# Performance work log

Measured on AMD Instinct MI355X. Metric: run time of the kernel, lower is better.

## Reference

```python
import jax, jax.numpy as jnp
import numpy as np

B, T, D, H = 2, 2048, 1024, 16
DH = D // H
PD = 6
SCALE = DH ** -0.5
_PAIRS4 = [(0, 1), (0, 2), (0, 3), (1, 2), (1, 3), (2, 3)]
_J6 = jnp.array([[0, 0, 0, 0, 0, 1], [0, 0, 0, 0, -1, 0], [0, 0, 0, 1, 0, 0],
                 [0, 0, 1, 0, 0, 0], [0, -1, 0, 0, 0, 0], [1, 0, 0, 0, 0, 0]], dtype=jnp.float32)


def exterior(p1, p2):
    # p1, p2: (..., 4) -> normalized 6-d Plucker line (..., 6)
    parts = [p1[..., i] * p2[..., j] - p1[..., j] * p2[..., i] for i, j in _PAIRS4]
    L = jnp.stack(parts, axis=-1)
    n = jnp.linalg.norm(L, axis=-1, keepdims=True)
    return L / jnp.clip(n, 1e-12)


def setup_inputs() -> dict:
    key = jax.random.key(0)
    ks = jax.random.split(key, 12)
    s = 0.02
    return {
        'x': jax.random.normal(ks[0], (B, T, D), jnp.float32),
        'qkv_w': jax.random.normal(ks[1], (D, 3 * D), jnp.float32) * s,
        'qkv_b': jnp.zeros((3 * D,), jnp.float32),
        'w1_write': jax.random.normal(ks[2], (D, 4 * H), jnp.float32) * s,
        'w2_write': jax.random.normal(ks[3], (D, 4 * H), jnp.float32) * s,
        'w1_read': jax.random.normal(ks[4], (D, 4 * H), jnp.float32) * s,
        'w2_read': jax.random.normal(ks[5], (D, 4 * H), jnp.float32) * s,
        'memv_w': jax.random.normal(ks[6], (D, D), jnp.float32) * s,
        'memv_b': jnp.zeros((D,), jnp.float32),
        'memg_w': jax.random.normal(ks[7], (D, H), jnp.float32) * s,
        'memg_b': jnp.zeros((H,), jnp.float32),
        'mem_scale': jnp.full((H,), 0.1, jnp.float32),
        'rw_mix': jnp.zeros((), jnp.float32),
        'out_w': jax.random.normal(ks[8], (D, D), jnp.float32) * s,
        'out_b': jnp.zeros((D,), jnp.float32),
        'decay_logits': jnp.full((H,), 4.6, jnp.float32),
    }


def reference(x, qkv_w, qkv_b, w1_write, w2_write, w1_read, w2_read,
              memv_w, memv_b, memg_w, memg_b, mem_scale, rw_mix,
              out_w, out_b, decay_logits):
    # ---- standard causal softmax attention ----
    qkv = (x @ qkv_w + qkv_b).reshape(B, T, 3, H, DH).transpose(2, 0, 3, 1, 4)
    q, k, v = qkv[0], qkv[1], qkv[2]                      # each (B,H,T,DH)
    scores = jnp.einsum('bhtd,bhsd->bhts', q, k) * SCALE
    mask = jnp.triu(jnp.ones((T, T), bool), 1)
    scores = jnp.where(mask[None, None], -jnp.inf, scores)
    attn = jax.nn.softmax(scores, axis=-1)                # dropout=0 (eval)
    seq_out = jnp.einsum('bhts,bhsd->bthd', attn, v).reshape(B, T, D)

    # ---- Plucker lines for write (prev->cur) and read ----
    x_prev = jnp.concatenate([jnp.zeros((B, 1, D), x.dtype), x[:, :-1]], axis=1)
    w1 = (x_prev @ w1_write).reshape(B, T, H, 4)
    w2 = (x @ w2_write).reshape(B, T, H, 4)
    write_lines = exterior(w1, w2)                        # (B,T,H,6)
    r1 = (x @ w1_read).reshape(B, T, H, 4)
    r2 = (x @ w2_read).reshape(B, T, H, 4)
    read_lines = exterior(r1, r2)

    Jw = jnp.einsum('bthi,ij->bhtj', write_lines, _J6)    # (B,H,T,6)
    Jr = jnp.einsum('bthi,ij->bhtj', read_lines, _J6)
    rd = read_lines.transpose(0, 2, 1, 3)                 # (B,H,T,6)

    # ---- decay-weighted cumsum of 6x6 outer-product states ----
    decays = jax.nn.sigmoid(decay_logits)                 # (H,)
    pos = jnp.arange(T, dtype=x.dtype)
    decay_inv = (1.0 / jnp.clip(decays, 1e-6))[:, None] ** pos[None]   # (H,T)
    decay_fwd = decays[:, None] ** pos[None]                           # (H,T)

    def shifted_state(Jv):
        outer = Jv[..., :, None] * Jv[..., None, :]       # (B,H,T,6,6)
        ow = outer * decay_inv[None, :, :, None, None]
        M = jnp.cumsum(ow, axis=2)
        M = jnp.concatenate([jnp.zeros((B, H, 1, PD, PD), x.dtype), M[:, :, :-1]], axis=2)
        return M * decay_fwd[None, :, :, None, None]

    Mw = shifted_state(Jw)
    Mr = shifted_state(Jr)

    score_w = jnp.einsum('bhti,bhtij,bhtj->bht', rd, Mw, rd)
    score_r = jnp.einsum('bhti,bhtij,bhtj->bht', Jw, Mr, Jw)
    alpha = jax.nn.sigmoid(rw_mix)
    mem_score = (1 - alpha) * score_w + alpha * score_r   # (B,H,T)

    mem_val = x @ memv_w + memv_b                         # (B,T,D)
    gate = jax.nn.sigmoid(x @ memg_w + memg_b)            # (B,T,H)
    mem_score_t = mem_score.transpose(0, 2, 1)            # (B,T,H)
    gated = jax.nn.sigmoid(mem_score_t * mem_scale[None, None, :]) * gate
    gated = gated.mean(axis=-1, keepdims=True)            # (B,T,1)

    return (seq_out + gated * mem_val) @ out_w + out_b
```

## Files before the change

### kernel.cpp

```cpp
#include <hip/hip_runtime.h>

#define Bb 2
#define Tt 2048
#define Dd 1024
#define Hh 16
#define LDC 4480

typedef __attribute__((ext_vector_type(8))) short s16x8;
typedef __attribute__((ext_vector_type(4))) float f32x4;
typedef __attribute__((ext_vector_type(8))) _Float16 f16x8;

__device__ __forceinline__ float bf2f(unsigned short u) {
  unsigned v = ((unsigned)u) << 16;
  union { unsigned u; float f; } c; c.u = v; return c.f;
}
__device__ __forceinline__ unsigned short f2bf(float f) {
  union { float f; unsigned u; } c; c.f = f;
  unsigned u = c.u + 0x7fffu + ((c.u >> 16) & 1u);
  return (unsigned short)(u >> 16);
}
__device__ __forceinline__ float sigm(float x) { return 1.f / (1.f + expf(-x)); }

__device__ __forceinline__ int swz(int row, int k) {
  return (k & ~31) | (k & 7) | (((((k >> 3) & 3) ^ ((row >> 1) & 3))) << 3);
}

__device__ __forceinline__ void async_copy16(void* lds, const void* g) {
  __builtin_amdgcn_global_load_lds(
      (const __attribute__((address_space(1))) unsigned int*)g,
      (__attribute__((address_space(3))) unsigned int*)lds, 16, 0, 0);
}


__global__ __launch_bounds__(256) void cast_x_kernel(const float* __restrict__ x,
                                                     unsigned short* __restrict__ xb) {
  int i = blockIdx.x * 256 + threadIdx.x;
  int row = i >> 7;
  int colbase = (i & 127) * 8;
  const float4* xv = reinterpret_cast<const float4*>(x + (size_t)i * 8);
  float4 a = xv[0], b = xv[1];
  s16x8 out;
  out[0] = (short)f2bf(a.x); out[1] = (short)f2bf(a.y);
  out[2] = (short)f2bf(a.z); out[3] = (short)f2bf(a.w);
  out[4] = (short)f2bf(b.x); out[5] = (short)f2bf(b.y);
  out[6] = (short)f2bf(b.z); out[7] = (short)f2bf(b.w);
  *(s16x8*)&xb[(size_t)row * 1024 + swz(row, colbase)] = out;
}


__global__ __launch_bounds__(256) void build_wt_kernel(const float* __restrict__ qkv_w,
                                                       const float* __restrict__ w1w,
                                                       const float* __restrict__ w2w,
                                                       const float* __restrict__ w1r,
                                                       const float* __restrict__ w2r,
                                                       const float* __restrict__ memg_w,
                                                       const float* __restrict__ memv_w,
                                                       unsigned short* __restrict__ WT) {
  __shared__ float tile[32][33];
  int n0 = blockIdx.x * 32, k0 = blockIdx.y * 32;
  int tx = threadIdx.x & 31, ty = threadIdx.x >> 5;
#pragma unroll
  for (int i = 0; i < 4; i++) {
    int k = k0 + ty + i * 8, n = n0 + tx;
    float v;
    if (n < 3072)       v = qkv_w[(size_t)k * 3072 + n];
    else if (n < 3136)  v = w1w[k * 64 + (n - 3072)];
    else if (n < 3200)  v = w2w[k * 64 + (n - 3136)];
    else if (n < 3264)  v = w1r[k * 64 + (n - 3200)];
    else if (n < 3328)  v = w2r[k * 64 + (n - 3264)];
    else if (n < 3344)  v = memg_w[k * 16 + (n - 3328)];
    else if (n < 3392)  v = 0.f;
    else if (n < 4416)  v = memv_w[(size_t)k * 1024 + (n - 3392)];
    else                v = 0.f;
    tile[ty + i * 8][tx] = v;
  }
  __syncthreads();
#pragma unroll
  for (int i = 0; i < 4; i++) {
    int n = n0 + ty + i * 8, k = k0 + tx;
    WT[(size_t)n * 1024 + swz(n, k)] = f2bf(tile[tx][ty + i * 8]);
  }
}

__global__ __launch_bounds__(256) void transpose_cast_kernel(const float* __restrict__ src,
                                                             int ncols,
                                                             unsigned short* __restrict__ dst) {
  __shared__ float tile[32][33];
  int n0 = blockIdx.x * 32, k0 = blockIdx.y * 32;
  int tx = threadIdx.x & 31, ty = threadIdx.x >> 5;
#pragma unroll
  for (int i = 0; i < 4; i++) {
    int k = k0 + ty + i * 8, n = n0 + tx;
    tile[ty + i * 8][tx] = (n < ncols) ? src[(size_t)k * ncols + n] : 0.f;
  }
  __syncthreads();
#pragma unroll
  for (int i = 0; i < 4; i++) {
    int n = n0 + ty + i * 8, k = k0 + tx;
    if (n < ncols) dst[(size_t)n * 1024 + swz(n, k)] = f2bf(tile[tx][ty + i * 8]);
  }
}

__global__ void bias_fill_kernel(const float* __restrict__ qkv_b,
                                 const float* __restrict__ memg_b,
                                 const float* __restrict__ memv_b,
                                 float* __restrict__ bias) {
  int i = blockIdx.x * 256 + threadIdx.x;
  if (i >= LDC) return;
  float v = 0.f;
  if (i < 3072) v = qkv_b[i];
  else if (i >= 3328 && i < 3344) v = memg_b[i - 3328];
  else if (i >= 3392 && i < 4416) v = memv_b[i - 3392];
  bias[i] = v;
}


template <bool OUT_BF16>
__global__ __launch_bounds__(256) void gemm_kernel(const unsigned short* __restrict__ A,
                                                   const unsigned short* __restrict__ Bt,
                                                   void* __restrict__ Cout,
                                                   const float* __restrict__ bias,
                                                   int M, int N, int K) {
  __shared__ unsigned short As[128 * 32];
  __shared__ unsigned short Bs[128 * 32];
  const int tid = threadIdx.x;
  const int lane = tid & 63, wid = tid >> 6;
  const int quad = lane >> 4, c16 = lane & 15;
  const int mBase = blockIdx.y * 128, nBase = blockIdx.x * 128;
  const int wm = wid >> 1, wn = wid & 1;
  const int srow = lane >> 2, scol = (lane & 3) << 3;
  const int slot = (quad ^ ((c16 >> 1) & 3)) * 8;

  f32x4 acc[4][4] = {};
  for (int k0 = 0; k0 < K; k0 += 32) {
    __syncthreads();
#pragma unroll
    for (int j = 0; j < 2; j++) {
      int rr = wid * 32 + j * 16;
      async_copy16(&As[rr * 32], &A[(size_t)(mBase + rr + srow) * K + k0 + scol]);
      async_copy16(&Bs[rr * 32], &Bt[(size_t)(nBase + rr + srow) * K + k0 + scol]);
    }
    __syncthreads();
    s16x8 af[4], bf[4];
#pragma unroll
    for (int mt = 0; mt < 4; mt++)
      af[mt] = *(const s16x8*)&As[(wm * 64 + mt * 16 + c16) * 32 + slot];
#pragma unroll
    for (int nt = 0; nt < 4; nt++)
      bf[nt] = *(const s16x8*)&Bs[(wn * 64 + nt * 16 + c16) * 32 + slot];
#pragma unroll
    for (int mt = 0; mt < 4; mt++)
#pragma unroll
      for (int nt = 0; nt < 4; nt++)
        acc[mt][nt] = __builtin_amdgcn_mfma_f32_16x16x32_bf16(af[mt], bf[nt], acc[mt][nt], 0, 0, 0);
  }
#pragma unroll
  for (int mt = 0; mt < 4; mt++)
#pragma unroll
    for (int nt = 0; nt < 4; nt++) {
      int col = nBase + wn * 64 + nt * 16 + c16;
      float bv = bias[col];
#pragma unroll
      for (int r = 0; r < 4; r++) {
        int row = mBase + wm * 64 + mt * 16 + quad * 4 + r;
        float v = acc[mt][nt][r] + bv;
        if (OUT_BF16)
          ((unsigned short*)Cout)[(size_t)row * N + col] = f2bf(v);
        else
          ((float*)Cout)[(size_t)row * N + col] = v;
      }
    }
}


__global__ __launch_bounds__(256) void repack_kernel(const unsigned short* __restrict__ Cq,
                                                     unsigned short* __restrict__ Kt,
                                                     unsigned short* __restrict__ Vt) {
  int kb = blockIdx.x & 63, bh = blockIdx.x >> 6;
  int b = bh >> 4, h = bh & 15;
  int tid = threadIdx.x;
  size_t tbase = ((size_t)bh * 64 + kb) * 2048;
  {
    int key = tid >> 3, p = tid & 7, dg = p ^ (key & 7);
    size_t src = (size_t)(b * Tt + kb * 32 + key) * LDC + 1024 + h * 64 + dg * 8;
    s16x8 kv = *(const s16x8*)&Cq[src];
    *(s16x8*)&Kt[tbase + (size_t)tid * 8] = kv;
  }
  __shared__ unsigned short vt[32 * 66];
  {
    int row = tid >> 3, c = tid & 7;
    size_t src = (size_t)(b * Tt + kb * 32 + row) * LDC + 2048 + h * 64 + c * 8;
    s16x8 vv = *(const s16x8*)&Cq[src];
#pragma unroll
    for (int e = 0; e < 8; e++) {
      union { _Float16 hf; unsigned short s; } cv;
      cv.hf = (_Float16)bf2f((unsigned short)vv[e]);
      vt[row * 66 + c * 8 + e] = cv.s;
    }
  }
  __syncthreads();
  {
    int d = tid >> 2, p = tid & 3, cq = p ^ ((d >> 2) & 3);
    s16x8 out;
#pragma unroll
    for (int e = 0; e < 8; e++) {
      int key = ((e >> 2) & 1) * 16 + cq * 4 + (e & 3);
      out[e] = (short)vt[key * 66 + d];
    }
    *(s16x8*)&Vt[tbase + (size_t)tid * 8] = out;
  }
}


__device__ __forceinline__ void do_tile(int ks, int q0, int quad, int c16,
                                        const s16x8& qf0, const s16x8& qf1,
                                        const s16x8 kf[2][2], const f16x8 vb[4],
                                        float& l_i, f32x4 o[4]) {
  f32x4 st0 = {}, st1 = {};
  st0 = __builtin_amdgcn_mfma_f32_16x16x32_bf16(kf[0][0], qf0, st0, 0, 0, 0);
  st0 = __builtin_amdgcn_mfma_f32_16x16x32_bf16(kf[0][1], qf1, st0, 0, 0, 0);
  st1 = __builtin_amdgcn_mfma_f32_16x16x32_bf16(kf[1][0], qf0, st1, 0, 0, 0);
  st1 = __builtin_amdgcn_mfma_f32_16x16x32_bf16(kf[1][1], qf1, st1, 0, 0, 0);
  bool need_mask = (ks + 31 > q0);
  f16x8 pa;
  float lp = 0.f;
#pragma unroll
  for (int r = 0; r < 4; r++) {
    float v0 = st0[r] * 0.125f;
    float v1 = st1[r] * 0.125f;
    if (need_mask) {
      v0 = (ks + quad * 4 + r      <= q0 + c16) ? v0 : -1e30f;
      v1 = (ks + 16 + quad * 4 + r <= q0 + c16) ? v1 : -1e30f;
    }
    float p0 = __expf(v0);
    float p1 = __expf(v1);
    lp += p0 + p1;
    pa[r]     = (_Float16)p0;
    pa[4 + r] = (_Float16)p1;
  }
  l_i += lp;
#pragma unroll
  for (int nt = 0; nt < 4; nt++)
    o[nt] = __builtin_amdgcn_mfma_f32_16x16x32_f16(pa, vb[nt], o[nt], 0, 0, 0);
}

__global__ __launch_bounds__(256) void attn_kernel(const unsigned short* __restrict__ Cq,
                                                   const unsigned short* __restrict__ Kt,
                                                   const unsigned short* __restrict__ Vt,
                                                   unsigned short* __restrict__ po) {
  __shared__ unsigned short Kl[2048];
  __shared__ unsigned short Vl[2048];
  const int g0 = blockIdx.x, bh = blockIdx.y;
  const int g = ((bh >> 4) & 1) ? (15 - g0) : g0;
  const int b = bh >> 4, h = bh & 15;
  const int w = threadIdx.x >> 6, lane = threadIdx.x & 63;
  const int quad = lane >> 4, c16 = lane & 15;
  const int pi = g * 4 + w;
  const int qA = pi * 16, qB = 2032 - pi * 16;
  const int nkA = qA + 16, nkB = 2048 - pi * 16;
  const int bound = 2048 - 64 * g;
  const unsigned short* Ktb = Kt + (size_t)bh * 64 * 2048;
  const unsigned short* Vtb = Vt + (size_t)bh * 64 * 2048;
  const int ci = threadIdx.x;

  size_t rowA = (size_t)(b * Tt + qA + c16) * LDC + h * 64;
  size_t rowB = (size_t)(b * Tt + qB + c16) * LDC + h * 64;
  s16x8 qA0 = *(const s16x8*)&Cq[rowA + quad * 8];
  s16x8 qA1 = *(const s16x8*)&Cq[rowA + 32 + quad * 8];
  s16x8 qB0 = *(const s16x8*)&Cq[rowB + quad * 8];
  s16x8 qB1 = *(const s16x8*)&Cq[rowB + 32 + quad * 8];

  float lA = 0.f, lB = 0.f;
  f32x4 oA[4] = {}, oB[4] = {};

  {
    s16x8 k0 = *(const s16x8*)&Ktb[(size_t)ci * 8];
    s16x8 v0 = *(const s16x8*)&Vtb[(size_t)ci * 8];
    *(s16x8*)&Kl[ci * 8] = k0;
    *(s16x8*)&Vl[ci * 8] = v0;
  }
  __syncthreads();

  for (int ks = 0; ks < bound; ks += 32) {
    bool more = (ks + 32) < bound;
    s16x8 kreg, vreg;
    if (more) {
      size_t nb = ((size_t)(ks >> 5) + 1) * 2048 + (size_t)ci * 8;
      kreg = *(const s16x8*)&Ktb[nb];
      vreg = *(const s16x8*)&Vtb[nb];
    }
    if (ks < nkB) {
      s16x8 kf[2][2];
#pragma unroll
      for (int gg = 0; gg < 2; gg++)
#pragma unroll
        for (int half = 0; half < 2; half++) {
          int key = gg * 16 + c16;
          int p = (half * 4 + quad) ^ (c16 & 7);
          kf[gg][half] = *(const s16x8*)&Kl[(key * 8 + p) * 8];
        }
      f16x8 vb[4];
#pragma unroll
      for (int nt = 0; nt < 4; nt++) {
        int d = nt * 16 + c16;
        int p = quad ^ ((d >> 2) & 3);
        vb[nt] = *(const f16x8*)&Vl[(d * 4 + p) * 8];
      }
      do_tile(ks, qB, quad, c16, qB0, qB1, kf, vb, lB, oB);
      if (ks < nkA)
        do_tile(ks, qA, quad, c16, qA0, qA1, kf, vb, lA, oA);
    }
    __syncthreads();
    if (more) {
      *(s16x8*)&Kl[ci * 8] = kreg;
      *(s16x8*)&Vl[ci * 8] = vreg;
      __syncthreads();
    }
  }

  lB += __shfl_xor(lB, 16, 64); lB += __shfl_xor(lB, 32, 64);
  lA += __shfl_xor(lA, 16, 64); lA += __shfl_xor(lA, 32, 64);
  float invB = 1.f / lB, invA = 1.f / lA;
#pragma unroll
  for (int r = 0; r < 4; r++) {
    float ivB = __shfl(invB, quad * 4 + r, 64);
    float ivA = __shfl(invA, quad * 4 + r, 64);
    size_t baseB = (size_t)(b * Tt + qB + quad * 4 + r) * Dd + h * 64;
    size_t baseA = (size_t)(b * Tt + qA + quad * 4 + r) * Dd + h * 64;
#pragma unroll
    for (int nt = 0; nt < 4; nt++) {
      po[baseB + nt * 16 + c16] = f2bf(oB[nt][r] * ivB);
      po[baseA + nt * 16 + c16] = f2bf(oA[nt][r] * ivA);
    }
  }
}


__device__ __forceinline__ void ext6(const float* p, const float* q, float* L) {
  L[0] = p[0] * q[1] - p[1] * q[0];
  L[1] = p[0] * q[2] - p[2] * q[0];
  L[2] = p[0] * q[3] - p[3] * q[0];
  L[3] = p[1] * q[2] - p[2] * q[1];
  L[4] = p[1] * q[3] - p[3] * q[1];
  L[5] = p[2] * q[3] - p[3] * q[2];
  float n = sqrtf(L[0]*L[0] + L[1]*L[1] + L[2]*L[2] + L[3]*L[3] + L[4]*L[4] + L[5]*L[5]);
  float inv = 1.f / fmaxf(n, 1e-12f);
#pragma unroll
  for (int k = 0; k < 6; k++) L[k] *= inv;
}

__global__ void lines_kernel(const unsigned short* __restrict__ Cq,
                             float* __restrict__ Jw, float* __restrict__ Jr,
                             float* __restrict__ rd) {
  int idx = blockIdx.x * 256 + threadIdx.x;
  int h = idx & 15, t = (idx >> 4) & 2047, b = idx >> 15;
  size_t row = (size_t)(b * Tt + t) * LDC;
  float w1[4], w2[4], r1[4], r2[4];
#pragma unroll
  for (int k = 0; k < 4; k++) {
    w1[k] = (t > 0) ? bf2f(Cq[row - LDC + 3072 + h * 4 + k]) : 0.f;
    w2[k] = bf2f(Cq[row + 3136 + h * 4 + k]);
    r1[k] = bf2f(Cq[row + 3200 + h * 4 + k]);
    r2[k] = bf2f(Cq[row + 3264 + h * 4 + k]);
  }
  float Lw[6], Lr[6];
  ext6(w1, w2, Lw);
  ext6(r1, r2, Lr);
  size_t ob = ((size_t)(b * Hh + h) * Tt + t) * 6;
  Jw[ob + 0] = Lw[5]; Jw[ob + 1] = -Lw[4]; Jw[ob + 2] = Lw[3];
  Jw[ob + 3] = Lw[2]; Jw[ob + 4] = -Lw[1]; Jw[ob + 5] = Lw[0];
  Jr[ob + 0] = Lr[5]; Jr[ob + 1] = -Lr[4]; Jr[ob + 2] = Lr[3];
  Jr[ob + 3] = Lr[2]; Jr[ob + 4] = -Lr[1]; Jr[ob + 5] = Lr[0];
#pragma unroll
  for (int k = 0; k < 6; k++) rd[ob + k] = Lr[k];
}


__global__ __launch_bounds__(64) void scanA_kernel(const float* __restrict__ Jw,
                                                   const float* __restrict__ Jr,
                                                   const float* __restrict__ decay_logits,
                                                   float* __restrict__ chunkA) {
  int blk = blockIdx.x;
  int chunk = blk & 15, bh = (blk >> 4) & 31, type = blk >> 9;
  int lane = threadIdx.x;
  const float* V = (type == 0 ? Jw : Jr) + ((size_t)bh * Tt + chunk * 128) * 6;
  __shared__ float v[768];
  for (int i = lane; i < 768; i += 64) v[i] = V[i];
  __syncthreads();
  float d = sigm(decay_logits[bh & 15]);
  int ll = lane < 36 ? lane : 35;
  int i6 = ll / 6, j6 = ll % 6;
  float A = 0.f;
  for (int s = 0; s < 128; s++) A = d * A + v[s * 6 + i6] * v[s * 6 + j6];
  if (lane < 36) chunkA[((size_t)(type * 32 + bh) * 16 + chunk) * 36 + lane] = A;
}

__global__ void scanA2_kernel(const float* __restrict__ chunkA,
                              const float* __restrict__ decay_logits,
                              float* __restrict__ Bst) {
  int idx = blockIdx.x * 256 + threadIdx.x;
  if (idx >= 2 * 32 * 36) return;
  int entry = idx % 36, bh = (idx / 36) % 32, type = idx / (36 * 32);
  float d = sigm(decay_logits[bh & 15]);
  float dS = powf(d, 128.f);
  float Bv = 0.f;
  size_t base = (size_t)(type * 32 + bh) * 16;
  for (int c = 0; c < 16; c++) {
    Bst[(base + c) * 36 + entry] = Bv;
    Bv = dS * Bv + d * chunkA[(base + c) * 36 + entry];
  }
}

__global__ __launch_bounds__(128) void scanB_kernel(const float* __restrict__ Jw,
                                                    const float* __restrict__ Jr,
                                                    const float* __restrict__ rd,
                                                    const float* __restrict__ Bst,
                                                    const float* __restrict__ decay_logits,
                                                    float* __restrict__ score_w,
                                                    float* __restrict__ score_r) {
  int blk = blockIdx.x;
  int chunk = blk & 15, bh = (blk >> 4) & 31, type = blk >> 9;
  int tl = threadIdx.x;
  size_t tb = ((size_t)bh * Tt + chunk * 128) * 6;
  const float* U = (type == 0 ? rd : Jw) + tb;
  const float* W = (type == 0 ? Jw : Jr) + tb;
  __shared__ float wv[768];
  __shared__ float Bm[36];
  for (int i = tl; i < 768; i += 128) wv[i] = W[i];
  if (tl < 36) Bm[tl] = Bst[((size_t)(type * 32 + bh) * 16 + chunk) * 36 + tl];
  __syncthreads();
  float d = sigm(decay_logits[bh & 15]);
  float u[6];
#pragma unroll
  for (int i = 0; i < 6; i++) u[i] = U[tl * 6 + i];
  float q = 0.f;
#pragma unroll
  for (int i = 0; i < 6; i++) {
    float bi = 0.f;
#pragma unroll
    for (int j = 0; j < 6; j++) bi += Bm[i * 6 + j] * u[j];
    q += u[i] * bi;
  }
  float acc = 0.f;
  for (int s = 0; s < tl; s++) {
    const float* ws = &wv[s * 6];
    float dot = u[0]*ws[0] + u[1]*ws[1] + u[2]*ws[2] + u[3]*ws[3] + u[4]*ws[4] + u[5]*ws[5];
    acc = d * (acc + dot * dot);
  }
  float score = acc + powf(d, (float)tl) * q;
  float* outp = (type == 0 ? score_w : score_r);
  outp[(size_t)bh * Tt + chunk * 128 + tl] = score;
}


__global__ __launch_bounds__(256) void combine_kernel(const unsigned short* __restrict__ po,
                                                      const unsigned short* __restrict__ Cq,
                                                      const float* __restrict__ score_w,
                                                      const float* __restrict__ score_r,
                                                      const float* __restrict__ mem_scale,
                                                      const float* __restrict__ rw_mix,
                                                      unsigned short* __restrict__ fused) {
  __shared__ float tmp[16];
  int rowi = blockIdx.x;
  int b = rowi >> 11, t = rowi & 2047;
  float alpha = sigm(rw_mix[0]);
  if (threadIdx.x < 16) {
    int h = threadIdx.x;
    size_t sh = (size_t)(b * 16 + h) * Tt + t;
    float ms = (1.f - alpha) * score_w[sh] + alpha * score_r[sh];
    float gate = sigm(bf2f(Cq[(size_t)rowi * LDC + 3328 + h]));
    tmp[h] = sigm(ms * mem_scale[h]) * gate;
  }
  __syncthreads();
  float g = 0.f;
#pragma unroll
  for (int h = 0; h < 16; h++) g += tmp[h];
  g *= (1.f / 16.f);
  for (int d = threadIdx.x; d < Dd; d += 256) {
    float sv = bf2f(po[((size_t)b * Tt + t) * Dd + d]);
    float mv = bf2f(Cq[(size_t)rowi * LDC + 3392 + d]);
    fused[(size_t)rowi * Dd + swz(rowi, d)] = f2bf(sv + g * mv);
  }
}


extern "C" void kernel_launch(void* const* d_in, const int* in_sizes, int n_in,
                              void* d_out, int out_size, void* d_ws, size_t ws_size,
                              hipStream_t stream) {
  (void)in_sizes; (void)n_in; (void)out_size; (void)ws_size;
  const float* x         = (const float*)d_in[0];
  const float* qkv_w     = (const float*)d_in[1];
  const float* qkv_b     = (const float*)d_in[2];
  const float* w1w       = (const float*)d_in[3];
  const float* w2w       = (const float*)d_in[4];
  const float* w1r       = (const float*)d_in[5];
  const float* w2r       = (const float*)d_in[6];
  const float* memv_w    = (const float*)d_in[7];
  const float* memv_b    = (const float*)d_in[8];
  const float* memg_w    = (const float*)d_in[9];
  const float* memg_b    = (const float*)d_in[10];
  const float* mem_scale = (const float*)d_in[11];
  const float* rw_mix    = (const float*)d_in[12];
  const float* out_w     = (const float*)d_in[13];
  const float* out_b     = (const float*)d_in[14];
  const float* decay_l   = (const float*)d_in[15];

  char* w = (char*)d_ws;
  unsigned short* xb    = (unsigned short*)(w + 0);
  unsigned short* Kt    = (unsigned short*)(w + 0);
  unsigned short* WT    = (unsigned short*)(w + 8388608);
  unsigned short* Vt    = (unsigned short*)(w + 8388608);
  unsigned short* outT  = (unsigned short*)(w + 17563648);
  float*          biasC = (float*)(w + 19660800);
  unsigned short* Cbuf  = (unsigned short*)(w + 19678720);
  unsigned short* po    = (unsigned short*)(w + 56378880);
  float*          Jw    = (float*)(w + 73680384);
  float*          Jr    = (float*)(w + 75253248);
  float*          rd    = (float*)(w + 76826112);
  float*          chA   = (float*)(w + 78398976);
  float*          Bst   = (float*)(w + 78546432);
  float*          sw    = (float*)(w + 78693888);
  float*          sr    = (float*)(w + 78956032);
  unsigned short* fused = (unsigned short*)(w + 79218176);

  cast_x_kernel<<<2048, 256, 0, stream>>>(x, xb);
  build_wt_kernel<<<dim3(140, 32), 256, 0, stream>>>(qkv_w, w1w, w2w, w1r, w2r,
                                                     memg_w, memv_w, WT);
  transpose_cast_kernel<<<dim3(32, 32), 256, 0, stream>>>(out_w, 1024, outT);
  bias_fill_kernel<<<18, 256, 0, stream>>>(qkv_b, memg_b, memv_b, biasC);

  gemm_kernel<true><<<dim3(35, 32), 256, 0, stream>>>(xb, WT, Cbuf, biasC, 4096, 4480, 1024);

  repack_kernel<<<2048, 256, 0, stream>>>(Cbuf, Kt, Vt);
  attn_kernel<<<dim3(16, 32), 256, 0, stream>>>(Cbuf, Kt, Vt, po);
  lines_kernel<<<256, 256, 0, stream>>>(Cbuf, Jw, Jr, rd);
  scanA_kernel<<<1024, 64, 0, stream>>>(Jw, Jr, decay_l, chA);
  scanA2_kernel<<<9, 256, 0, stream>>>(chA, decay_l, Bst);
  scanB_kernel<<<1024, 128, 0, stream>>>(Jw, Jr, rd, Bst, decay_l, sw, sr);
  combine_kernel<<<4096, 256, 0, stream>>>(po, Cbuf, sw, sr, mem_scale, rw_mix, fused);

  gemm_kernel<false><<<dim3(8, 32), 256, 0, stream>>>(fused, outT, d_out, out_b, 4096, 1024, 1024);
}
```

Baseline: 299.4 us.

## Merge prep/post kernels, fold chunk scan into scanB, retile GEMMs

Merges the four preprocessing kernels into one prep_kernel and the repack and lines kernels into one post1_kernel. scanA2 is removed: each scanB block recomputes its chunk prefix state serially from chunkA. The main GEMM now loads K in 64-wide steps across two LDS buffers and remaps block indices for grouped L2 locality. The output GEMM uses 64-row tiles so more blocks are launched. The aim is fewer launches, fewer barriers per K step and better occupancy, at the cost of redundant prefix work in scanB and more LDS per block.

```diff
diff --git a/kernel.cpp b/kernel.cpp
--- a/kernel.cpp
+++ b/kernel.cpp
@@ -32,127 +32,140 @@
 }
 
 
-__global__ __launch_bounds__(256) void cast_x_kernel(const float* __restrict__ x,
-                                                     unsigned short* __restrict__ xb) {
-  int i = blockIdx.x * 256 + threadIdx.x;
-  int row = i >> 7;
-  int colbase = (i & 127) * 8;
-  const float4* xv = reinterpret_cast<const float4*>(x + (size_t)i * 8);
-  float4 a = xv[0], b = xv[1];
-  s16x8 out;
-  out[0] = (short)f2bf(a.x); out[1] = (short)f2bf(a.y);
-  out[2] = (short)f2bf(a.z); out[3] = (short)f2bf(a.w);
-  out[4] = (short)f2bf(b.x); out[5] = (short)f2bf(b.y);
-  out[6] = (short)f2bf(b.z); out[7] = (short)f2bf(b.w);
-  *(s16x8*)&xb[(size_t)row * 1024 + swz(row, colbase)] = out;
-}
-
-
-__global__ __launch_bounds__(256) void build_wt_kernel(const float* __restrict__ qkv_w,
-                                                       const float* __restrict__ w1w,
-                                                       const float* __restrict__ w2w,
-                                                       const float* __restrict__ w1r,
-                                                       const float* __restrict__ w2r,
-                                                       const float* __restrict__ memg_w,
-                                                       const float* __restrict__ memv_w,
-                                                       unsigned short* __restrict__ WT) {
+__global__ __launch_bounds__(256) void prep_kernel(const float* __restrict__ x,
+                                                   const float* __restrict__ qkv_w,
+                                                   const float* __restrict__ w1w,
+                                                   const float* __restrict__ w2w,
+                                                   const float* __restrict__ w1r,
+                                                   const float* __restrict__ w2r,
+                                                   const float* __restrict__ memg_w,
+                                                   const float* __restrict__ memv_w,
+                                                   const float* __restrict__ out_w,
+                                                   const float* __restrict__ qkv_b,
+                                                   const float* __restrict__ memg_b,
+                                                   const float* __restrict__ memv_b,
+                                                   unsigned short* __restrict__ xb,
+                                                   unsigned short* __restrict__ WT,
+                                                   unsigned short* __restrict__ outT,
+                                                   float* __restrict__ biasC) {
   __shared__ float tile[32][33];
-  int n0 = blockIdx.x * 32, k0 = blockIdx.y * 32;
-  int tx = threadIdx.x & 31, ty = threadIdx.x >> 5;
-#pragma unroll
-  for (int i = 0; i < 4; i++) {
-    int k = k0 + ty + i * 8, n = n0 + tx;
-    float v;
-    if (n < 3072)       v = qkv_w[(size_t)k * 3072 + n];
-    else if (n < 3136)  v = w1w[k * 64 + (n - 3072)];
-    else if (n < 3200)  v = w2w[k * 64 + (n - 3136)];
-    else if (n < 3264)  v = w1r[k * 64 + (n - 3200)];
-    else if (n < 3328)  v = w2r[k * 64 + (n - 3264)];
-    else if (n < 3344)  v = memg_w[k * 16 + (n - 3328)];
-    else if (n < 3392)  v = 0.f;
-    else if (n < 4416)  v = memv_w[(size_t)k * 1024 + (n - 3392)];
-    else                v = 0.f;
-    tile[ty + i * 8][tx] = v;
-  }
-  __syncthreads();
-#pragma unroll
-  for (int i = 0; i < 4; i++) {
-    int n = n0 + ty + i * 8, k = k0 + tx;
-    WT[(size_t)n * 1024 + swz(n, k)] = f2bf(tile[tx][ty + i * 8]);
-  }
-}
-
-__global__ __launch_bounds__(256) void transpose_cast_kernel(const float* __restrict__ src,
-                                                             int ncols,
-                                                             unsigned short* __restrict__ dst) {
-  __shared__ float tile[32][33];
-  int n0 = blockIdx.x * 32, k0 = blockIdx.y * 32;
-  int tx = threadIdx.x & 31, ty = threadIdx.x >> 5;
-#pragma unroll
-  for (int i = 0; i < 4; i++) {
-    int k = k0 + ty + i * 8, n = n0 + tx;
-    tile[ty + i * 8][tx] = (n < ncols) ? src[(size_t)k * ncols + n] : 0.f;
-  }
-  __syncthreads();
-#pragma unroll
-  for (int i = 0; i < 4; i++) {
-    int n = n0 + ty + i * 8, k = k0 + tx;
-    if (n < ncols) dst[(size_t)n * 1024 + swz(n, k)] = f2bf(tile[tx][ty + i * 8]);
-  }
-}
-
-__global__ void bias_fill_kernel(const float* __restrict__ qkv_b,
-                                 const float* __restrict__ memg_b,
-                                 const float* __restrict__ memv_b,
-                                 float* __restrict__ bias) {
-  int i = blockIdx.x * 256 + threadIdx.x;
-  if (i >= LDC) return;
-  float v = 0.f;
-  if (i < 3072) v = qkv_b[i];
-  else if (i >= 3328 && i < 3344) v = memg_b[i - 3328];
-  else if (i >= 3392 && i < 4416) v = memv_b[i - 3392];
-  bias[i] = v;
-}
-
-
-template <bool OUT_BF16>
+  int id = blockIdx.x;
+  if (id < 2048) {
+    int i = id * 256 + threadIdx.x;
+    int row = i >> 7;
+    int colbase = (i & 127) * 8;
+    const float4* xv = reinterpret_cast<const float4*>(x + (size_t)i * 8);
+    float4 a = xv[0], b = xv[1];
+    s16x8 out;
+    out[0] = (short)f2bf(a.x); out[1] = (short)f2bf(a.y);
+    out[2] = (short)f2bf(a.z); out[3] = (short)f2bf(a.w);
+    out[4] = (short)f2bf(b.x); out[5] = (short)f2bf(b.y);
+    out[6] = (short)f2bf(b.z); out[7] = (short)f2bf(b.w);
+    *(s16x8*)&xb[(size_t)row * 1024 + swz(row, colbase)] = out;
+  } else if (id < 6528) {
+    int j = id - 2048;
+    int n0 = (j % 140) * 32, k0 = (j / 140) * 32;
+    int tx = threadIdx.x & 31, ty = threadIdx.x >> 5;
+#pragma unroll
+    for (int i = 0; i < 4; i++) {
+      int k = k0 + ty + i * 8, n = n0 + tx;
+      float v;
+      if (n < 3072)       v = qkv_w[(size_t)k * 3072 + n];
+      else if (n < 3136)  v = w1w[k * 64 + (n - 3072)];
+      else if (n < 3200)  v = w2w[k * 64 + (n - 3136)];
+      else if (n < 3264)  v = w1r[k * 64 + (n - 3200)];
+      else if (n < 3328)  v = w2r[k * 64 + (n - 3264)];
+      else if (n < 3344)  v = memg_w[k * 16 + (n - 3328)];
+      else if (n < 3392)  v = 0.f;
+      else if (n < 4416)  v = memv_w[(size_t)k * 1024 + (n - 3392)];
+      else                v = 0.f;
+      tile[ty + i * 8][tx] = v;
+    }
+    __syncthreads();
+#pragma unroll
+    for (int i = 0; i < 4; i++) {
+      int n = n0 + ty + i * 8, k = k0 + tx;
+      WT[(size_t)n * 1024 + swz(n, k)] = f2bf(tile[tx][ty + i * 8]);
+    }
+  } else if (id < 7552) {
+    int j = id - 6528;
+    int n0 = (j & 31) * 32, k0 = (j >> 5) * 32;
+    int tx = threadIdx.x & 31, ty = threadIdx.x >> 5;
+#pragma unroll
+    for (int i = 0; i < 4; i++) {
+      int k = k0 + ty + i * 8, n = n0 + tx;
+      tile[ty + i * 8][tx] = out_w[(size_t)k * 1024 + n];
+    }
+    __syncthreads();
+#pragma unroll
+    for (int i = 0; i < 4; i++) {
+      int n = n0 + ty + i * 8, k = k0 + tx;
+      outT[(size_t)n * 1024 + swz(n, k)] = f2bf(tile[tx][ty + i * 8]);
+    }
+  } else {
+    int i = (id - 7552) * 256 + threadIdx.x;
+    if (i < LDC) {
+      float v = 0.f;
+      if (i < 3072) v = qkv_b[i];
+      else if (i >= 3328 && i < 3344) v = memg_b[i - 3328];
+      else if (i >= 3392 && i < 4416) v = memv_b[i - 3392];
+      biasC[i] = v;
+    }
+  }
+}
+
+
 __global__ __launch_bounds__(256) void gemm_kernel(const unsigned short* __restrict__ A,
                                                    const unsigned short* __restrict__ Bt,
-                                                   void* __restrict__ Cout,
-                                                   const float* __restrict__ bias,
-                                                   int M, int N, int K) {
-  __shared__ unsigned short As[128 * 32];
-  __shared__ unsigned short Bs[128 * 32];
+                                                   unsigned short* __restrict__ Cout,
+                                                   const float* __restrict__ bias) {
+  const int K = 1024;
+  const int x = blockIdx.x & 7, local = blockIdx.x >> 3;
+  const int mTile = (x >> 1) * 8 + (local & 7);
+  const int nTile = (x & 1) * 18 + (local >> 3);
+  if (nTile >= 35) return;
+  const int mBase = mTile * 128, nBase = nTile * 128;
+
+  __shared__ unsigned short As0[128 * 32], As1[128 * 32];
+  __shared__ unsigned short Bs0[128 * 32], Bs1[128 * 32];
   const int tid = threadIdx.x;
   const int lane = tid & 63, wid = tid >> 6;
   const int quad = lane >> 4, c16 = lane & 15;
-  const int mBase = blockIdx.y * 128, nBase = blockIdx.x * 128;
   const int wm = wid >> 1, wn = wid & 1;
   const int srow = lane >> 2, scol = (lane & 3) << 3;
   const int slot = (quad ^ ((c16 >> 1) & 3)) * 8;
 
   f32x4 acc[4][4] = {};
-  for (int k0 = 0; k0 < K; k0 += 32) {
+  for (int k0 = 0; k0 < K; k0 += 64) {
     __syncthreads();
 #pragma unroll
     for (int j = 0; j < 2; j++) {
       int rr = wid * 32 + j * 16;
-      async_copy16(&As[rr * 32], &A[(size_t)(mBase + rr + srow) * K + k0 + scol]);
-      async_copy16(&Bs[rr * 32], &Bt[(size_t)(nBase + rr + srow) * K + k0 + scol]);
-    }
-    __syncthreads();
-    s16x8 af[4], bf[4];
-#pragma unroll
-    for (int mt = 0; mt < 4; mt++)
-      af[mt] = *(const s16x8*)&As[(wm * 64 + mt * 16 + c16) * 32 + slot];
-#pragma unroll
-    for (int nt = 0; nt < 4; nt++)
-      bf[nt] = *(const s16x8*)&Bs[(wn * 64 + nt * 16 + c16) * 32 + slot];
-#pragma unroll
-    for (int mt = 0; mt < 4; mt++)
+      size_t ga = (size_t)(mBase + rr + srow) * K + k0 + scol;
+      size_t gb = (size_t)(nBase + rr + srow) * K + k0 + scol;
+      async_copy16(&As0[rr * 32], &A[ga]);
+      async_copy16(&Bs0[rr * 32], &Bt[gb]);
+      async_copy16(&As1[rr * 32], &A[ga + 32]);
+      async_copy16(&Bs1[rr * 32], &Bt[gb + 32]);
+    }
+    __syncthreads();
+#pragma unroll
+    for (int kk = 0; kk < 2; kk++) {
+      const unsigned short* Asp = kk ? As1 : As0;
+      const unsigned short* Bsp = kk ? Bs1 : Bs0;
+      s16x8 af[4], bf[4];
+#pragma unroll
+      for (int mt = 0; mt < 4; mt++)
+        af[mt] = *(const s16x8*)&Asp[(wm * 64 + mt * 16 + c16) * 32 + slot];
 #pragma unroll
       for (int nt = 0; nt < 4; nt++)
-        acc[mt][nt] = __builtin_amdgcn_mfma_f32_16x16x32_bf16(af[mt], bf[nt], acc[mt][nt], 0, 0, 0);
+        bf[nt] = *(const s16x8*)&Bsp[(wn * 64 + nt * 16 + c16) * 32 + slot];
+#pragma unroll
+      for (int mt = 0; mt < 4; mt++)
+#pragma unroll
+        for (int nt = 0; nt < 4; nt++)
+          acc[mt][nt] = __builtin_amdgcn_mfma_f32_16x16x32_bf16(af[mt], bf[nt], acc[mt][nt], 0, 0, 0);
+    }
   }
 #pragma unroll
   for (int mt = 0; mt < 4; mt++)
@@ -163,51 +176,154 @@
 #pragma unroll
       for (int r = 0; r < 4; r++) {
         int row = mBase + wm * 64 + mt * 16 + quad * 4 + r;
-        float v = acc[mt][nt][r] + bv;
-        if (OUT_BF16)
-          ((unsigned short*)Cout)[(size_t)row * N + col] = f2bf(v);
-        else
-          ((float*)Cout)[(size_t)row * N + col] = v;
+        Cout[(size_t)row * 4480 + col] = f2bf(acc[mt][nt][r] + bv);
       }
     }
 }
 
 
-__global__ __launch_bounds__(256) void repack_kernel(const unsigned short* __restrict__ Cq,
-                                                     unsigned short* __restrict__ Kt,
-                                                     unsigned short* __restrict__ Vt) {
-  int kb = blockIdx.x & 63, bh = blockIdx.x >> 6;
-  int b = bh >> 4, h = bh & 15;
+__global__ __launch_bounds__(256) void gemm_out_kernel(const unsigned short* __restrict__ A,
+                                                       const unsigned short* __restrict__ Bt,
+                                                       float* __restrict__ Cout,
+                                                       const float* __restrict__ bias) {
+  const int K = 1024;
+  const int mBase = blockIdx.y * 64, nBase = blockIdx.x * 128;
+  __shared__ unsigned short As0[64 * 32], As1[64 * 32];
+  __shared__ unsigned short Bs0[128 * 32], Bs1[128 * 32];
+  const int tid = threadIdx.x;
+  const int lane = tid & 63, wid = tid >> 6;
+  const int quad = lane >> 4, c16 = lane & 15;
+  const int wm = wid >> 1, wn = wid & 1;
+  const int srow = lane >> 2, scol = (lane & 3) << 3;
+  const int slot = (quad ^ ((c16 >> 1) & 3)) * 8;
+
+  f32x4 acc[2][4] = {};
+  for (int k0 = 0; k0 < K; k0 += 64) {
+    __syncthreads();
+    {
+      int rrA = wid * 16;
+      size_t ga = (size_t)(mBase + rrA + srow) * K + k0 + scol;
+      async_copy16(&As0[rrA * 32], &A[ga]);
+      async_copy16(&As1[rrA * 32], &A[ga + 32]);
+#pragma unroll
+      for (int j = 0; j < 2; j++) {
+        int rr = wid * 32 + j * 16;
+        size_t gb = (size_t)(nBase + rr + srow) * K + k0 + scol;
+        async_copy16(&Bs0[rr * 32], &Bt[gb]);
+        async_copy16(&Bs1[rr * 32], &Bt[gb + 32]);
+      }
+    }
+    __syncthreads();
+#pragma unroll
+    for (int kk = 0; kk < 2; kk++) {
+      const unsigned short* Asp = kk ? As1 : As0;
+      const unsigned short* Bsp = kk ? Bs1 : Bs0;
+      s16x8 af[2], bf[4];
+#pragma unroll
+      for (int mt = 0; mt < 2; mt++)
+        af[mt] = *(const s16x8*)&Asp[(wm * 32 + mt * 16 + c16) * 32 + slot];
+#pragma unroll
+      for (int nt = 0; nt < 4; nt++)
+        bf[nt] = *(const s16x8*)&Bsp[(wn * 64 + nt * 16 + c16) * 32 + slot];
+#pragma unroll
+      for (int mt = 0; mt < 2; mt++)
+#pragma unroll
+        for (int nt = 0; nt < 4; nt++)
+          acc[mt][nt] = __builtin_amdgcn_mfma_f32_16x16x32_bf16(af[mt], bf[nt], acc[mt][nt], 0, 0, 0);
+    }
+  }
+#pragma unroll
+  for (int mt = 0; mt < 2; mt++)
+#pragma unroll
+    for (int nt = 0; nt < 4; nt++) {
+      int col = nBase + wn * 64 + nt * 16 + c16;
+      float bv = bias[col];
+#pragma unroll
+      for (int r = 0; r < 4; r++) {
+        int row = mBase + wm * 32 + mt * 16 + quad * 4 + r;
+        Cout[(size_t)row * 1024 + col] = acc[mt][nt][r] + bv;
+      }
+    }
+}
+
+
+__device__ __forceinline__ void ext6(const float* p, const float* q, float* L) {
+  L[0] = p[0] * q[1] - p[1] * q[0];
+  L[1] = p[0] * q[2] - p[2] * q[0];
+  L[2] = p[0] * q[3] - p[3] * q[0];
+  L[3] = p[1] * q[2] - p[2] * q[1];
+  L[4] = p[1] * q[3] - p[3] * q[1];
+  L[5] = p[2] * q[3] - p[3] * q[2];
+  float n = sqrtf(L[0]*L[0] + L[1]*L[1] + L[2]*L[2] + L[3]*L[3] + L[4]*L[4] + L[5]*L[5]);
+  float inv = 1.f / fmaxf(n, 1e-12f);
+#pragma unroll
+  for (int k = 0; k < 6; k++) L[k] *= inv;
+}
+
+
+__global__ __launch_bounds__(256) void post1_kernel(const unsigned short* __restrict__ Cq,
+                                                    unsigned short* __restrict__ Kt,
+                                                    unsigned short* __restrict__ Vt,
+                                                    float* __restrict__ Jw,
+                                                    float* __restrict__ Jr,
+                                                    float* __restrict__ rd) {
+  __shared__ unsigned short vt[32 * 66];
+  int id = blockIdx.x;
   int tid = threadIdx.x;
-  size_t tbase = ((size_t)bh * 64 + kb) * 2048;
-  {
-    int key = tid >> 3, p = tid & 7, dg = p ^ (key & 7);
-    size_t src = (size_t)(b * Tt + kb * 32 + key) * LDC + 1024 + h * 64 + dg * 8;
-    s16x8 kv = *(const s16x8*)&Cq[src];
-    *(s16x8*)&Kt[tbase + (size_t)tid * 8] = kv;
-  }
-  __shared__ unsigned short vt[32 * 66];
-  {
-    int row = tid >> 3, c = tid & 7;
-    size_t src = (size_t)(b * Tt + kb * 32 + row) * LDC + 2048 + h * 64 + c * 8;
-    s16x8 vv = *(const s16x8*)&Cq[src];
-#pragma unroll
-    for (int e = 0; e < 8; e++) {
-      union { _Float16 hf; unsigned short s; } cv;
-      cv.hf = (_Float16)bf2f((unsigned short)vv[e]);
-      vt[row * 66 + c * 8 + e] = cv.s;
-    }
-  }
-  __syncthreads();
-  {
-    int d = tid >> 2, p = tid & 3, cq = p ^ ((d >> 2) & 3);
-    s16x8 out;
-#pragma unroll
-    for (int e = 0; e < 8; e++) {
-      int key = ((e >> 2) & 1) * 16 + cq * 4 + (e & 3);
-      out[e] = (short)vt[key * 66 + d];
-    }
-    *(s16x8*)&Vt[tbase + (size_t)tid * 8] = out;
+  if (id < 2048) {
+    int kb = id & 63, bh = id >> 6;
+    int b = bh >> 4, h = bh & 15;
+    size_t tbase = ((size_t)bh * 64 + kb) * 2048;
+    {
+      int key = tid >> 3, p = tid & 7, dg = p ^ (key & 7);
+      size_t src = (size_t)(b * Tt + kb * 32 + key) * LDC + 1024 + h * 64 + dg * 8;
+      s16x8 kv = *(const s16x8*)&Cq[src];
+      *(s16x8*)&Kt[tbase + (size_t)tid * 8] = kv;
+    }
+    {
+      int row = tid >> 3, c = tid & 7;
+      size_t src = (size_t)(b * Tt + kb * 32 + row) * LDC + 2048 + h * 64 + c * 8;
+      s16x8 vv = *(const s16x8*)&Cq[src];
+#pragma unroll
+      for (int e = 0; e < 8; e++) {
+        union { _Float16 hf; unsigned short s; } cv;
+        cv.hf = (_Float16)bf2f((unsigned short)vv[e]);
+        vt[row * 66 + c * 8 + e] = cv.s;
+      }
+    }
+    __syncthreads();
+    {
+      int d = tid >> 2, p = tid & 3, cq = p ^ ((d >> 2) & 3);
+      s16x8 out;
+#pragma unroll
+      for (int e = 0; e < 8; e++) {
+        int key = ((e >> 2) & 1) * 16 + cq * 4 + (e & 3);
+        out[e] = (short)vt[key * 66 + d];
+      }
+      *(s16x8*)&Vt[tbase + (size_t)tid * 8] = out;
+    }
+  } else {
+    int idx = (id - 2048) * 256 + tid;
+    int h = idx & 15, t = (idx >> 4) & 2047, b = idx >> 15;
+    size_t row = (size_t)(b * Tt + t) * LDC;
+    float w1[4], w2[4], r1[4], r2[4];
+#pragma unroll
+    for (int k = 0; k < 4; k++) {
+      w1[k] = (t > 0) ? bf2f(Cq[row - LDC + 3072 + h * 4 + k]) : 0.f;
+      w2[k] = bf2f(Cq[row + 3136 + h * 4 + k]);
+      r1[k] = bf2f(Cq[row + 3200 + h * 4 + k]);
+      r2[k] = bf2f(Cq[row + 3264 + h * 4 + k]);
+    }
+    float Lw[6], Lr[6];
+    ext6(w1, w2, Lw);
+    ext6(r1, r2, Lr);
+    size_t ob = ((size_t)(b * Hh + h) * Tt + t) * 6;
+    Jw[ob + 0] = Lw[5]; Jw[ob + 1] = -Lw[4]; Jw[ob + 2] = Lw[3];
+    Jw[ob + 3] = Lw[2]; Jw[ob + 4] = -Lw[1]; Jw[ob + 5] = Lw[0];
+    Jr[ob + 0] = Lr[5]; Jr[ob + 1] = -Lr[4]; Jr[ob + 2] = Lr[3];
+    Jr[ob + 3] = Lr[2]; Jr[ob + 4] = -Lr[1]; Jr[ob + 5] = Lr[0];
+#pragma unroll
+    for (int k = 0; k < 6; k++) rd[ob + k] = Lr[k];
   }
 }
 
@@ -336,46 +452,6 @@
 }
 
 
-__device__ __forceinline__ void ext6(const float* p, const float* q, float* L) {
-  L[0] = p[0] * q[1] - p[1] * q[0];
-  L[1] = p[0] * q[2] - p[2] * q[0];
-  L[2] = p[0] * q[3] - p[3] * q[0];
-  L[3] = p[1] * q[2] - p[2] * q[1];
-  L[4] = p[1] * q[3] - p[3] * q[1];
-  L[5] = p[2] * q[3] - p[3] * q[2];
-  float n = sqrtf(L[0]*L[0] + L[1]*L[1] + L[2]*L[2] + L[3]*L[3] + L[4]*L[4] + L[5]*L[5]);
-  float inv = 1.f / fmaxf(n, 1e-12f);
-#pragma unroll
-  for (int k = 0; k < 6; k++) L[k] *= inv;
-}
-
-__global__ void lines_kernel(const unsigned short* __restrict__ Cq,
-                             float* __restrict__ Jw, float* __restrict__ Jr,
-                             float* __restrict__ rd) {
-  int idx = blockIdx.x * 256 + threadIdx.x;
-  int h = idx & 15, t = (idx >> 4) & 2047, b = idx >> 15;
-  size_t row = (size_t)(b * Tt + t) * LDC;
-  float w1[4], w2[4], r1[4], r2[4];
-#pragma unroll
-  for (int k = 0; k < 4; k++) {
-    w1[k] = (t > 0) ? bf2f(Cq[row - LDC + 3072 + h * 4 + k]) : 0.f;
-    w2[k] = bf2f(Cq[row + 3136 + h * 4 + k]);
-    r1[k] = bf2f(Cq[row + 3200 + h * 4 + k]);
-    r2[k] = bf2f(Cq[row + 3264 + h * 4 + k]);
-  }
-  float Lw[6], Lr[6];
-  ext6(w1, w2, Lw);
-  ext6(r1, r2, Lr);
-  size_t ob = ((size_t)(b * Hh + h) * Tt + t) * 6;
-  Jw[ob + 0] = Lw[5]; Jw[ob + 1] = -Lw[4]; Jw[ob + 2] = Lw[3];
-  Jw[ob + 3] = Lw[2]; Jw[ob + 4] = -Lw[1]; Jw[ob + 5] = Lw[0];
-  Jr[ob + 0] = Lr[5]; Jr[ob + 1] = -Lr[4]; Jr[ob + 2] = Lr[3];
-  Jr[ob + 3] = Lr[2]; Jr[ob + 4] = -Lr[1]; Jr[ob + 5] = Lr[0];
-#pragma unroll
-  for (int k = 0; k < 6; k++) rd[ob + k] = Lr[k];
-}
-
-
 __global__ __launch_bounds__(64) void scanA_kernel(const float* __restrict__ Jw,
                                                    const float* __restrict__ Jr,
                                                    const float* __restrict__ decay_logits,
@@ -395,26 +471,11 @@
   if (lane < 36) chunkA[((size_t)(type * 32 + bh) * 16 + chunk) * 36 + lane] = A;
 }
 
-__global__ void scanA2_kernel(const float* __restrict__ chunkA,
-                              const float* __restrict__ decay_logits,
-                              float* __restrict__ Bst) {
-  int idx = blockIdx.x * 256 + threadIdx.x;
-  if (idx >= 2 * 32 * 36) return;
-  int entry = idx % 36, bh = (idx / 36) % 32, type = idx / (36 * 32);
-  float d = sigm(decay_logits[bh & 15]);
-  float dS = powf(d, 128.f);
-  float Bv = 0.f;
-  size_t base = (size_t)(type * 32 + bh) * 16;
-  for (int c = 0; c < 16; c++) {
-    Bst[(base + c) * 36 + entry] = Bv;
-    Bv = dS * Bv + d * chunkA[(base + c) * 36 + entry];
-  }
-}
 
 __global__ __launch_bounds__(128) void scanB_kernel(const float* __restrict__ Jw,
                                                     const float* __restrict__ Jr,
                                                     const float* __restrict__ rd,
-                                                    const float* __restrict__ Bst,
+                                                    const float* __restrict__ chunkA,
                                                     const float* __restrict__ decay_logits,
                                                     float* __restrict__ score_w,
                                                     float* __restrict__ score_r) {
@@ -427,9 +488,16 @@
   __shared__ float wv[768];
   __shared__ float Bm[36];
   for (int i = tl; i < 768; i += 128) wv[i] = W[i];
-  if (tl < 36) Bm[tl] = Bst[((size_t)(type * 32 + bh) * 16 + chunk) * 36 + tl];
+  float d = sigm(decay_logits[bh & 15]);
+  if (tl < 36) {
+    float dS = powf(d, 128.f);
+    float Bv = 0.f;
+    size_t base = (size_t)(type * 32 + bh) * 16;
+    for (int c = 0; c < chunk; c++)
+      Bv = dS * Bv + d * chunkA[(base + c) * 36 + tl];
+    Bm[tl] = Bv;
+  }
   __syncthreads();
-  float d = sigm(decay_logits[bh & 15]);
   float u[6];
 #pragma unroll
   for (int i = 0; i < 6; i++) u[i] = U[tl * 6 + i];
@@ -518,26 +586,21 @@
   float*          Jr    = (float*)(w + 75253248);
   float*          rd    = (float*)(w + 76826112);
   float*          chA   = (float*)(w + 78398976);
-  float*          Bst   = (float*)(w + 78546432);
   float*          sw    = (float*)(w + 78693888);
   float*          sr    = (float*)(w + 78956032);
   unsigned short* fused = (unsigned short*)(w + 79218176);
 
-  cast_x_kernel<<<2048, 256, 0, stream>>>(x, xb);
-  build_wt_kernel<<<dim3(140, 32), 256, 0, stream>>>(qkv_w, w1w, w2w, w1r, w2r,
-                                                     memg_w, memv_w, WT);
-  transpose_cast_kernel<<<dim3(32, 32), 256, 0, stream>>>(out_w, 1024, outT);
-  bias_fill_kernel<<<18, 256, 0, stream>>>(qkv_b, memg_b, memv_b, biasC);
-
-  gemm_kernel<true><<<dim3(35, 32), 256, 0, stream>>>(xb, WT, Cbuf, biasC, 4096, 4480, 1024);
-
-  repack_kernel<<<2048, 256, 0, stream>>>(Cbuf, Kt, Vt);
+  prep_kernel<<<7570, 256, 0, stream>>>(x, qkv_w, w1w, w2w, w1r, w2r, memg_w, memv_w,
+                                        out_w, qkv_b, memg_b, memv_b,
+                                        xb, WT, outT, biasC);
+
+  gemm_kernel<<<1152, 256, 0, stream>>>(xb, WT, Cbuf, biasC);
+
+  post1_kernel<<<2304, 256, 0, stream>>>(Cbuf, Kt, Vt, Jw, Jr, rd);
   attn_kernel<<<dim3(16, 32), 256, 0, stream>>>(Cbuf, Kt, Vt, po);
-  lines_kernel<<<256, 256, 0, stream>>>(Cbuf, Jw, Jr, rd);
   scanA_kernel<<<1024, 64, 0, stream>>>(Jw, Jr, decay_l, chA);
-  scanA2_kernel<<<9, 256, 0, stream>>>(chA, decay_l, Bst);
-  scanB_kernel<<<1024, 128, 0, stream>>>(Jw, Jr, rd, Bst, decay_l, sw, sr);
+  scanB_kernel<<<1024, 128, 0, stream>>>(Jw, Jr, rd, chA, decay_l, sw, sr);
   combine_kernel<<<4096, 256, 0, stream>>>(po, Cbuf, sw, sr, mem_scale, rw_mix, fused);
 
-  gemm_kernel<false><<<dim3(8, 32), 256, 0, stream>>>(fused, outT, d_out, out_b, 4096, 1024, 1024);
-}
+  gemm_out_kernel<<<dim3(8, 64), 256, 0, stream>>>(fused, outT, (float*)d_out, out_b);
+}
```

Result: faster. 283.8 us (-5.2%).
